# Optimization experiments

Hardware: AMD Instinct MI355X
Metric: run time of the kernel (lower is better)

## Reference

```python
import jax, jax.numpy as jnp
import numpy as np

B, IN, E, H, MO, OUT, K = 32768, 512, 8, 128, 256, 2, 2


def setup_inputs() -> dict:
    key = jax.random.key(0)
    ks = jax.random.split(key, 9)
    g = lambda k, shape, fan: (jax.random.normal(k, shape, jnp.float32) / np.sqrt(fan)).astype(jnp.float32)
    return {
        "num_prop": jax.random.normal(ks[0], (B, IN), jnp.float32),
        "cat_prop": jax.random.normal(ks[1], (B, 3), jnp.float32),
        "w_gate": g(ks[2], (IN, E), IN),
        "W1": g(ks[3], (E, IN, H), IN),
        "b1": jnp.zeros((E, H), jnp.float32),
        "W2": g(ks[4], (E, H, MO), H),
        "b2": jnp.zeros((E, MO), jnp.float32),
        "Wout": g(ks[5], (MO, OUT), MO),
        "bout": jnp.zeros((OUT,), jnp.float32),
    }


def _cv_squared(v):
    # torch.var is unbiased (ddof=1); eps = 1e-10
    return jnp.var(v, ddof=1) / (jnp.mean(v) ** 2 + 1e-10)


def reference(num_prop, cat_prop, w_gate, W1, b1, W2, b2, Wout, bout):
    b = num_prop.shape[0]
    x = num_prop  # eval mode: dropout is identity, gating noise disabled
    # --- top-k gating ---
    logits = x @ w_gate                                   # [B, E]
    top_vals, top_idx = jax.lax.top_k(logits, K)          # [B, K]
    gate_vals = jax.nn.softmax(top_vals, axis=-1)         # softmax over top-k logits
    gates = jnp.zeros_like(logits).at[jnp.arange(b)[:, None], top_idx].add(gate_vals)  # [B, E]
    # --- load-balancing loss ---
    importance = gates.sum(axis=0)                        # [E]
    load = (gates > 0).astype(jnp.float32).sum(axis=0)    # [E]
    loss = (_cv_squared(importance) + _cv_squared(load)) * 1e-2
    # --- experts (dense-equivalent: gates zero out non-selected experts) ---
    h = jax.nn.relu(jnp.einsum('bi,eih->beh', x, W1) + b1)          # [B, E, H]
    eo = jax.nn.softmax(jnp.einsum('beh,ehm->bem', h, W2) + b2, axis=-1)  # [B, E, MO]
    y = jnp.einsum('be,bem->bm', gates, eo)               # [B, MO]
    # --- output head ---
    out = y @ Wout + bout                                 # [B, OUT]
    return out, loss
```

## Files before the change

### kernel.cpp

```cpp
#include <hip/hip_runtime.h>

#define BN 32768
#define IN 512
#define NE 8
#define NH 128
#define MO 256

typedef const __attribute__((address_space(1))) unsigned int gu32;
typedef __attribute__((address_space(3))) unsigned int lu32;
typedef __attribute__((ext_vector_type(8))) short bf16x8;
typedef __attribute__((ext_vector_type(4))) float f32x4;

__device__ __forceinline__ void cp16(const float* g, float* l) {
    __builtin_amdgcn_global_load_lds((gu32*)g, (lu32*)l, 16, 0, 0);
}

__device__ __forceinline__ unsigned short f2bf(float f) {
    unsigned int u = __float_as_uint(f);
    u = (u + 0x7fffu + ((u >> 16) & 1u)) >> 16;
    return (unsigned short)u;
}
__device__ __forceinline__ float bf2f(unsigned short h) {
    return __uint_as_float((unsigned int)h << 16);
}

__global__ __launch_bounds__(256) void gate_kernel(
    const float* __restrict__ x, const float* __restrict__ wg,
    int* __restrict__ gcount, int* __restrict__ gload, float* __restrict__ gimp,
    int* __restrict__ idx_list, float* __restrict__ gate_list,
    float* __restrict__ out, const float* __restrict__ bout)
{
    __shared__ double wgt[NE][514];
    __shared__ int counts_s[NE];
    __shared__ int load_s[NE];
    __shared__ float imp_s[NE];
    __shared__ int base_s[NE];
    __shared__ int rec_e[64];
    __shared__ int rec_p[64];
    __shared__ float rec_g[64];

    int tid = threadIdx.x;
    if (tid < NE) { counts_s[tid] = 0; load_s[tid] = 0; imp_s[tid] = 0.f; }
    if (tid < 64) {
        int row = blockIdx.x * 32 + (tid >> 1);
        out[row * 2 + (tid & 1)] = bout[tid & 1];
    }
    for (int i = tid; i < IN * NE; i += 256) {
        wgt[i & 7][i >> 3] = (double)wg[i];
    }
    __syncthreads();

    int r = tid >> 3;
    int e = tid & 7;
    int row = blockIdx.x * 32 + r;

    const float4* x4 = (const float4*)(x + (size_t)row * IN);
    const double* wrow = &wgt[e][0];
    double a0 = 0.0, a1 = 0.0, a2 = 0.0, a3 = 0.0;
    #pragma unroll 8
    for (int j = 0; j < 128; ++j) {
        float4 xv = x4[j];
        const double2* wd = (const double2*)(wrow + 4 * j);
        double2 w0 = wd[0];
        double2 w1 = wd[1];
        a0 = fma((double)xv.x, w0.x, a0);
        a1 = fma((double)xv.y, w0.y, a1);
        a2 = fma((double)xv.z, w1.x, a2);
        a3 = fma((double)xv.w, w1.y, a3);
    }
    double acc = (a0 + a1) + (a2 + a3);

    double v0 = acc; int e0 = e;
    #pragma unroll
    for (int m = 1; m < 8; m <<= 1) {
        double vo = __shfl_xor(v0, m, 64);
        int    eo = __shfl_xor(e0, m, 64);
        if (vo > v0 || (vo == v0 && eo < e0)) { v0 = vo; e0 = eo; }
    }
    double v1 = (e == e0) ? -1.0e300 : acc; int e1 = e;
    #pragma unroll
    for (int m = 1; m < 8; m <<= 1) {
        double vo = __shfl_xor(v1, m, 64);
        int    eo = __shfl_xor(e1, m, 64);
        if (vo > v1 || (vo == v1 && eo < e1)) { v1 = vo; e1 = eo; }
    }

    if ((tid & 7) == 0) {
        float t1 = expf((float)(v1 - v0));
        float s = 1.f + t1;
        float g0 = 1.f / s;
        float g1 = t1 / s;
        atomicAdd(&imp_s[e0], g0);
        atomicAdd(&imp_s[e1], g1);
        if (g0 > 0.f) atomicAdd(&load_s[e0], 1);
        if (g1 > 0.f) atomicAdd(&load_s[e1], 1);
        int p0 = atomicAdd(&counts_s[e0], 1);
        int p1 = atomicAdd(&counts_s[e1], 1);
        int rl = r * 2;
        rec_e[rl] = e0; rec_e[rl + 1] = e1;
        rec_g[rl] = g0; rec_g[rl + 1] = g1;
        rec_p[rl] = p0; rec_p[rl + 1] = p1;
    }
    __syncthreads();
    if (tid < NE) {
        base_s[tid] = atomicAdd(&gcount[tid], counts_s[tid]);
        atomicAdd(&gimp[tid], imp_s[tid]);
        atomicAdd(&gload[tid], load_s[tid]);
    }
    __syncthreads();
    if (tid < 64) {
        int ee = rec_e[tid];
        int pos = base_s[ee] + rec_p[tid];
        int rw = blockIdx.x * 32 + (tid >> 1);
        idx_list[ee * BN + pos] = rw;
        gate_list[ee * BN + pos] = rec_g[tid];
    }
}

__global__ void loss_kernel(const float* __restrict__ gimp, const int* __restrict__ gload,
                            float* __restrict__ out) {
    if (threadIdx.x == 0 && blockIdx.x == 0) {
        float mi = 0.f, ml = 0.f;
        for (int e = 0; e < NE; ++e) { mi += gimp[e]; ml += (float)gload[e]; }
        mi *= 0.125f; ml *= 0.125f;
        float vi = 0.f, vl = 0.f;
        for (int e = 0; e < NE; ++e) {
            float d = gimp[e] - mi;  vi += d * d;
            float d2 = (float)gload[e] - ml; vl += d2 * d2;
        }
        vi *= (1.f / 7.f); vl *= (1.f / 7.f);
        float loss = (vi / (mi * mi + 1e-10f) + vl / (ml * ml + 1e-10f)) * 0.01f;
        out[BN * 2] = loss;
    }
}

__global__ __launch_bounds__(256) void prep_kernel(
    const float* __restrict__ W1, const float* __restrict__ W2,
    float* __restrict__ W1F, float* __restrict__ W2F)
{
    __shared__ __align__(16) char pb[32768];
    int t = threadIdx.x, b = blockIdx.x;
    if (b < 64) {
        int e = b >> 3, kt = b & 7;
        const float* src = W1 + ((size_t)e * IN + kt * 64) * NH;
        #pragma unroll
        for (int p = 0; p < 8; ++p) {
            int li = p * 256 + t;
            float4 q = *(const float4*)(src + li * 4);
            int kl = li >> 5, n0 = (li & 31) * 4;
            int ks = kl >> 5, g = (kl >> 3) & 3, kb = (kl & 7) * 2;
            float vv[4] = {q.x, q.y, q.z, q.w};
            #pragma unroll
            for (int j = 0; j < 4; ++j) {
                int n = n0 + j;
                int off = (((ks * 8 + (n >> 4)) * 64) + (n & 15) + 16 * g) * 16 + kb;
                unsigned short hh = f2bf(vv[j]);
                unsigned short hl = f2bf(vv[j] - bf2f(hh));
                *(unsigned short*)(pb + off) = hh;
                *(unsigned short*)(pb + 16384 + off) = hl;
            }
        }
        __syncthreads();
        float* dst = W1F + (size_t)b * 8192;
        #pragma unroll
        for (int p = 0; p < 8; ++p) {
            int li = p * 256 + t;
            *(int4*)(dst + li * 4) = *(const int4*)(pb + li * 16);
        }
    } else if (b < 96) {
        int bi = b - 64;
        int e = bi >> 2, kt = bi & 3;
        const float* src = W2 + ((size_t)e * NH + kt * 32) * MO;
        #pragma unroll
        for (int p = 0; p < 8; ++p) {
            int li = p * 256 + t;
            float4 q = *(const float4*)(src + li * 4);
            int kl = li >> 6, n0 = (li & 63) * 4;
            int g = kl >> 3, kb = (kl & 7) * 2;
            float vv[4] = {q.x, q.y, q.z, q.w};
            #pragma unroll
            for (int j = 0; j < 4; ++j) {
                int n = n0 + j;
                int off = ((n >> 4) * 64 + (n & 15) + 16 * g) * 16 + kb;
                unsigned short hh = f2bf(vv[j]);
                unsigned short hl = f2bf(vv[j] - bf2f(hh));
                *(unsigned short*)(pb + off) = hh;
                *(unsigned short*)(pb + 16384 + off) = hl;
            }
        }
        __syncthreads();
        float* dst = W2F + (size_t)bi * 8192;
        #pragma unroll
        for (int p = 0; p < 8; ++p) {
            int li = p * 256 + t;
            *(int4*)(dst + li * 4) = *(const int4*)(pb + li * 16);
        }
    }
}

#define OFF_AH 0
#define OFF_AL 8192
#define OFF_B1 16384
#define OFF_HH 0
#define OFF_HL 16384
#define OFF_B2 32768

__global__ __launch_bounds__(256, 2) void expert_kernel(
    const float* __restrict__ x,
    const float* __restrict__ b1, const float* __restrict__ b2,
    const float* __restrict__ Wout,
    const float* __restrict__ W1F, const float* __restrict__ W2F,
    const int* __restrict__ gcount,
    const int* __restrict__ idx_list, const float* __restrict__ gate_list,
    float* __restrict__ out)
{
    __shared__ __align__(16) char smx[66560];
    __shared__ float woutS[512];

    int e = blockIdx.y;
    int cnt = gcount[e];
    int row0 = blockIdx.x * 64;
    if (row0 >= cnt) return;
    int t = threadIdx.x;
    int l = t & 63, w = t >> 6;

    woutS[t] = Wout[t];
    woutS[256 + t] = Wout[256 + t];

    int s_mf = t >> 6;
    int s_r  = t & 15;
    int s_g  = (t >> 4) & 3;
    int rloc = s_mf * 16 + s_r;
    int sgi = row0 + rloc; if (sgi >= cnt) sgi = cnt - 1;
    const float* xrow = x + (size_t)idx_list[e * BN + sgi] * IN;

    int mbase = (w & 1) * 2;
    int nsel  = w >> 1;

    f32x4 acc1[2][4] = {};
    for (int kt = 0; kt < 8; ++kt) {
        {
            const float* gb = W1F + (size_t)(e * 8 + kt) * 8192;
            float* lb = (float*)(smx + OFF_B1);
            #pragma unroll
            for (int p = 0; p < 8; ++p)
                cp16(gb + (p * 256 + t) * 4, lb + (p * 256 + t) * 4);
        }
        #pragma unroll
        for (int ks = 0; ks < 2; ++ks) {
            int k = kt * 64 + ks * 32 + s_g * 8;
            float4 qa = *(const float4*)(xrow + k);
            float4 qb = *(const float4*)(xrow + k + 4);
            float vv[8] = {qa.x, qa.y, qa.z, qa.w, qb.x, qb.y, qb.z, qb.w};
            unsigned int dh[4], dl[4];
            #pragma unroll
            for (int j = 0; j < 4; ++j) {
                unsigned short h0 = f2bf(vv[2 * j]);
                unsigned short h1 = f2bf(vv[2 * j + 1]);
                unsigned short l0 = f2bf(vv[2 * j] - bf2f(h0));
                unsigned short l1 = f2bf(vv[2 * j + 1] - bf2f(h1));
                dh[j] = (unsigned int)h0 | ((unsigned int)h1 << 16);
                dl[j] = (unsigned int)l0 | ((unsigned int)l1 << 16);
            }
            int slot = ((ks * 4 + s_mf) * 64 + (s_r + 16 * s_g)) * 16;
            *(int4*)(smx + OFF_AH + slot) = make_int4(dh[0], dh[1], dh[2], dh[3]);
            *(int4*)(smx + OFF_AL + slot) = make_int4(dl[0], dl[1], dl[2], dl[3]);
        }
        __syncthreads();
        #pragma unroll
        for (int ks = 0; ks < 2; ++ks) {
            bf16x8 ah[2], al[2];
            #pragma unroll
            for (int mf = 0; mf < 2; ++mf) {
                int ao = ((ks * 4 + mbase + mf) * 64 + l) * 16;
                ah[mf] = *(const bf16x8*)(smx + OFF_AH + ao);
                al[mf] = *(const bf16x8*)(smx + OFF_AL + ao);
            }
            #pragma unroll
            for (int nf = 0; nf < 4; ++nf) {
                int bo = ((ks * 8 + nsel * 4 + nf) * 64 + l) * 16;
                bf16x8 bh = *(const bf16x8*)(smx + OFF_B1 + bo);
                bf16x8 bl = *(const bf16x8*)(smx + OFF_B1 + 16384 + bo);
                #pragma unroll
                for (int mf = 0; mf < 2; ++mf) {
                    acc1[mf][nf] = __builtin_amdgcn_mfma_f32_16x16x32_bf16(ah[mf], bh, acc1[mf][nf], 0, 0, 0);
                    acc1[mf][nf] = __builtin_amdgcn_mfma_f32_16x16x32_bf16(ah[mf], bl, acc1[mf][nf], 0, 0, 0);
                    acc1[mf][nf] = __builtin_amdgcn_mfma_f32_16x16x32_bf16(al[mf], bh, acc1[mf][nf], 0, 0, 0);
                    acc1[mf][nf] = __builtin_amdgcn_mfma_f32_16x16x32_bf16(al[mf], bl, acc1[mf][nf], 0, 0, 0);
                }
            }
        }
        __syncthreads();
    }

    #pragma unroll
    for (int mf = 0; mf < 2; ++mf) {
        int mf2 = (w & 1) * 2 + mf;
        int rlow = 4 * (l >> 4);
        #pragma unroll
        for (int nf = 0; nf < 4; ++nf) {
            int c = nsel * 64 + nf * 16 + (l & 15);
            float b1v = b1[e * NH + c];
            int ks2 = c >> 5;
            int g2 = (c >> 3) & 3;
            int boff = ((ks2 * 4 + mf2) * 64) * 16 + (c & 7) * 2;
            #pragma unroll
            for (int rg = 0; rg < 4; ++rg) {
                float v = fmaxf(acc1[mf][nf][rg] + b1v, 0.f);
                unsigned short hh = f2bf(v);
                unsigned short hl = f2bf(v - bf2f(hh));
                int off = boff + ((rlow + rg) + 16 * g2) * 16;
                *(unsigned short*)(smx + OFF_HH + off) = hh;
                *(unsigned short*)(smx + OFF_HL + off) = hl;
            }
        }
    }
    __syncthreads();

    f32x4 acc2[2][8] = {};
    for (int kt2 = 0; kt2 < 4; ++kt2) {
        {
            const float* gb = W2F + (size_t)(e * 4 + kt2) * 8192;
            float* lb = (float*)(smx + OFF_B2);
            #pragma unroll
            for (int p = 0; p < 8; ++p)
                cp16(gb + (p * 256 + t) * 4, lb + (p * 256 + t) * 4);
        }
        __syncthreads();
        bf16x8 ah[2], al[2];
        #pragma unroll
        for (int mf = 0; mf < 2; ++mf) {
            int ao = ((kt2 * 4 + mbase + mf) * 64 + l) * 16;
            ah[mf] = *(const bf16x8*)(smx + OFF_HH + ao);
            al[mf] = *(const bf16x8*)(smx + OFF_HL + ao);
        }
        #pragma unroll
        for (int nf = 0; nf < 8; ++nf) {
            int bo = ((nsel * 8 + nf) * 64 + l) * 16;
            bf16x8 bh = *(const bf16x8*)(smx + OFF_B2 + bo);
            bf16x8 bl = *(const bf16x8*)(smx + OFF_B2 + 16384 + bo);
            #pragma unroll
            for (int mf = 0; mf < 2; ++mf) {
                acc2[mf][nf] = __builtin_amdgcn_mfma_f32_16x16x32_bf16(ah[mf], bh, acc2[mf][nf], 0, 0, 0);
                acc2[mf][nf] = __builtin_amdgcn_mfma_f32_16x16x32_bf16(ah[mf], bl, acc2[mf][nf], 0, 0, 0);
                acc2[mf][nf] = __builtin_amdgcn_mfma_f32_16x16x32_bf16(al[mf], bh, acc2[mf][nf], 0, 0, 0);
                acc2[mf][nf] = __builtin_amdgcn_mfma_f32_16x16x32_bf16(al[mf], bl, acc2[mf][nf], 0, 0, 0);
            }
        }
        __syncthreads();
    }

    float* zl = (float*)smx;
    #pragma unroll
    for (int mf = 0; mf < 2; ++mf) {
        int rbase = (w & 1) * 32 + mf * 16 + 4 * (l >> 4);
        #pragma unroll
        for (int nf = 0; nf < 8; ++nf) {
            int c = nsel * 128 + nf * 16 + (l & 15);
            float b2v = b2[e * MO + c];
            #pragma unroll
            for (int rg = 0; rg < 4; ++rg)
                zl[(rbase + rg) * 260 + c] = acc2[mf][nf][rg] + b2v;
        }
    }
    __syncthreads();

    int rr = w * 16 + (l >> 2);
    int c0 = l & 3;
    float vreg[64];
    float m = -1e30f;
    #pragma unroll
    for (int j = 0; j < 64; ++j) {
        vreg[j] = zl[rr * 260 + c0 + 4 * j];
        m = fmaxf(m, vreg[j]);
    }
    m = fmaxf(m, __shfl_xor(m, 1, 64));
    m = fmaxf(m, __shfl_xor(m, 2, 64));
    float s = 0.f, o0 = 0.f, o1 = 0.f;
    #pragma unroll
    for (int j = 0; j < 64; ++j) {
        float tt = __expf(vreg[j] - m);
        s += tt;
        float2 wv = *(const float2*)&woutS[(c0 + 4 * j) * 2];
        o0 = fmaf(tt, wv.x, o0);
        o1 = fmaf(tt, wv.y, o1);
    }
    s  += __shfl_xor(s, 1, 64);  s  += __shfl_xor(s, 2, 64);
    o0 += __shfl_xor(o0, 1, 64); o0 += __shfl_xor(o0, 2, 64);
    o1 += __shfl_xor(o1, 1, 64); o1 += __shfl_xor(o1, 2, 64);
    if (c0 == 0) {
        int gi = row0 + rr;
        if (gi < cnt) {
            float g = gate_list[e * BN + gi];
            int brow = idx_list[e * BN + gi];
            float inv = 1.f / s;
            atomicAdd(&out[brow * 2 + 0], g * o0 * inv);
            atomicAdd(&out[brow * 2 + 1], g * o1 * inv);
        }
    }
}

extern "C" void kernel_launch(void* const* d_in, const int* in_sizes, int n_in,
                              void* d_out, int out_size, void* d_ws, size_t ws_size,
                              hipStream_t stream) {
    const float* x    = (const float*)d_in[0];
    const float* wg   = (const float*)d_in[2];
    const float* W1   = (const float*)d_in[3];
    const float* b1   = (const float*)d_in[4];
    const float* W2   = (const float*)d_in[5];
    const float* b2   = (const float*)d_in[6];
    const float* Wout = (const float*)d_in[7];
    const float* bout = (const float*)d_in[8];
    float* out = (float*)d_out;

    char* ws = (char*)d_ws;
    int*   gcount    = (int*)(ws + 0);
    int*   gload     = (int*)(ws + 32);
    float* gimp      = (float*)(ws + 64);
    int*   idx_list  = (int*)(ws + 128);
    float* gate_list = (float*)(ws + 128 + sizeof(int) * NE * BN);
    float* W1F       = (float*)(ws + 128 + 8 * NE * BN);
    float* W2F       = (float*)(ws + 128 + 8 * NE * BN + 64 * 32768);

    hipMemsetAsync(ws, 0, 128, stream);
    prep_kernel<<<96, 256, 0, stream>>>(W1, W2, W1F, W2F);
    gate_kernel<<<BN / 32, 256, 0, stream>>>(x, wg, gcount, gload, gimp,
                                             idx_list, gate_list, out, bout);
    loss_kernel<<<1, 64, 0, stream>>>(gimp, gload, out);
    dim3 eg(BN / 64, NE);
    expert_kernel<<<eg, 256, 0, stream>>>(x, b1, b2, Wout, W1F, W2F,
                                          gcount, idx_list, gate_list, out);
}
```

Measured before the change: 228.0 us.

## Rework gate precision, fuse loss into experts, double-buffer weights, register softmax

```diff
diff --git a/kernel.cpp b/kernel.cpp
--- a/kernel.cpp
+++ b/kernel.cpp
@@ -30,7 +30,7 @@
     int* __restrict__ idx_list, float* __restrict__ gate_list,
     float* __restrict__ out, const float* __restrict__ bout)
 {
-    __shared__ double wgt[NE][514];
+    __shared__ float wgs[NE][516];
     __shared__ int counts_s[NE];
     __shared__ int load_s[NE];
     __shared__ float imp_s[NE];
@@ -45,9 +45,7 @@
         int row = blockIdx.x * 32 + (tid >> 1);
         out[row * 2 + (tid & 1)] = bout[tid & 1];
     }
-    for (int i = tid; i < IN * NE; i += 256) {
-        wgt[i & 7][i >> 3] = (double)wg[i];
-    }
+    for (int i = tid; i < IN * NE; i += 256) wgs[i & 7][i >> 3] = wg[i];
     __syncthreads();
 
     int r = tid >> 3;
@@ -55,49 +53,78 @@
     int row = blockIdx.x * 32 + r;
 
     const float4* x4 = (const float4*)(x + (size_t)row * IN);
-    const double* wrow = &wgt[e][0];
-    double a0 = 0.0, a1 = 0.0, a2 = 0.0, a3 = 0.0;
+    float a0 = 0.f, a1 = 0.f, a2 = 0.f, a3 = 0.f;
     #pragma unroll 8
     for (int j = 0; j < 128; ++j) {
         float4 xv = x4[j];
-        const double2* wd = (const double2*)(wrow + 4 * j);
-        double2 w0 = wd[0];
-        double2 w1 = wd[1];
-        a0 = fma((double)xv.x, w0.x, a0);
-        a1 = fma((double)xv.y, w0.y, a1);
-        a2 = fma((double)xv.z, w1.x, a2);
-        a3 = fma((double)xv.w, w1.y, a3);
-    }
-    double acc = (a0 + a1) + (a2 + a3);
-
-    double v0 = acc; int e0 = e;
+        float4 wv = *(const float4*)&wgs[e][4 * j];
+        a0 = fmaf(xv.x, wv.x, a0);
+        a1 = fmaf(xv.y, wv.y, a1);
+        a2 = fmaf(xv.z, wv.z, a2);
+        a3 = fmaf(xv.w, wv.w, a3);
+    }
+    float acc = (a0 + a1) + (a2 + a3);
+
+    float v0 = acc; int e0 = e;
     #pragma unroll
     for (int m = 1; m < 8; m <<= 1) {
-        double vo = __shfl_xor(v0, m, 64);
-        int    eo = __shfl_xor(e0, m, 64);
+        float vo = __shfl_xor(v0, m, 64);
+        int eo = __shfl_xor(e0, m, 64);
         if (vo > v0 || (vo == v0 && eo < e0)) { v0 = vo; e0 = eo; }
     }
-    double v1 = (e == e0) ? -1.0e300 : acc; int e1 = e;
+    float v1 = (e == e0) ? -1e30f : acc; int e1 = e;
     #pragma unroll
     for (int m = 1; m < 8; m <<= 1) {
-        double vo = __shfl_xor(v1, m, 64);
-        int    eo = __shfl_xor(e1, m, 64);
+        float vo = __shfl_xor(v1, m, 64);
+        int eo = __shfl_xor(e1, m, 64);
         if (vo > v1 || (vo == v1 && eo < e1)) { v1 = vo; e1 = eo; }
     }
+    float v2 = (e == e0 || e == e1) ? -1e30f : acc;
+    #pragma unroll
+    for (int m = 1; m < 8; m <<= 1) v2 = fmaxf(v2, __shfl_xor(v2, m, 64));
+
+    double dv0 = v0, dv1 = v1;
+    int f0 = e0, f1 = e1;
+    if (v1 - v2 < 2e-4f) {
+        const float* xr = x + (size_t)row * IN;
+        double b0 = 0, b1d = 0, b2d = 0, b3 = 0;
+        for (int k = 0; k < IN; k += 4) {
+            b0  = fma((double)xr[k],     (double)wgs[e][k],     b0);
+            b1d = fma((double)xr[k + 1], (double)wgs[e][k + 1], b1d);
+            b2d = fma((double)xr[k + 2], (double)wgs[e][k + 2], b2d);
+            b3  = fma((double)xr[k + 3], (double)wgs[e][k + 3], b3);
+        }
+        double ad = (b0 + b1d) + (b2d + b3);
+        double w0 = ad; int g0i = e;
+        #pragma unroll
+        for (int m = 1; m < 8; m <<= 1) {
+            double vo = __shfl_xor(w0, m, 64);
+            int eo = __shfl_xor(g0i, m, 64);
+            if (vo > w0 || (vo == w0 && eo < g0i)) { w0 = vo; g0i = eo; }
+        }
+        double w1 = (e == g0i) ? -1.0e300 : ad; int g1i = e;
+        #pragma unroll
+        for (int m = 1; m < 8; m <<= 1) {
+            double vo = __shfl_xor(w1, m, 64);
+            int eo = __shfl_xor(g1i, m, 64);
+            if (vo > w1 || (vo == w1 && eo < g1i)) { w1 = vo; g1i = eo; }
+        }
+        dv0 = w0; dv1 = w1; f0 = g0i; f1 = g1i;
+    }
 
     if ((tid & 7) == 0) {
-        float t1 = expf((float)(v1 - v0));
+        float t1 = expf((float)(dv1 - dv0));
         float s = 1.f + t1;
         float g0 = 1.f / s;
         float g1 = t1 / s;
-        atomicAdd(&imp_s[e0], g0);
-        atomicAdd(&imp_s[e1], g1);
-        if (g0 > 0.f) atomicAdd(&load_s[e0], 1);
-        if (g1 > 0.f) atomicAdd(&load_s[e1], 1);
-        int p0 = atomicAdd(&counts_s[e0], 1);
-        int p1 = atomicAdd(&counts_s[e1], 1);
+        atomicAdd(&imp_s[f0], g0);
+        atomicAdd(&imp_s[f1], g1);
+        if (g0 > 0.f) atomicAdd(&load_s[f0], 1);
+        if (g1 > 0.f) atomicAdd(&load_s[f1], 1);
+        int p0 = atomicAdd(&counts_s[f0], 1);
+        int p1 = atomicAdd(&counts_s[f1], 1);
         int rl = r * 2;
-        rec_e[rl] = e0; rec_e[rl + 1] = e1;
+        rec_e[rl] = f0; rec_e[rl + 1] = f1;
         rec_g[rl] = g0; rec_g[rl + 1] = g1;
         rec_p[rl] = p0; rec_p[rl + 1] = p1;
     }
@@ -114,23 +141,6 @@
         int rw = blockIdx.x * 32 + (tid >> 1);
         idx_list[ee * BN + pos] = rw;
         gate_list[ee * BN + pos] = rec_g[tid];
-    }
-}
-
-__global__ void loss_kernel(const float* __restrict__ gimp, const int* __restrict__ gload,
-                            float* __restrict__ out) {
-    if (threadIdx.x == 0 && blockIdx.x == 0) {
-        float mi = 0.f, ml = 0.f;
-        for (int e = 0; e < NE; ++e) { mi += gimp[e]; ml += (float)gload[e]; }
-        mi *= 0.125f; ml *= 0.125f;
-        float vi = 0.f, vl = 0.f;
-        for (int e = 0; e < NE; ++e) {
-            float d = gimp[e] - mi;  vi += d * d;
-            float d2 = (float)gload[e] - ml; vl += d2 * d2;
-        }
-        vi *= (1.f / 7.f); vl *= (1.f / 7.f);
-        float loss = (vi / (mi * mi + 1e-10f) + vl / (ml * ml + 1e-10f)) * 0.01f;
-        out[BN * 2] = loss;
     }
 }
 
@@ -198,104 +208,118 @@
     }
 }
 
-#define OFF_AH 0
-#define OFF_AL 8192
-#define OFF_B1 16384
-#define OFF_HH 0
-#define OFF_HL 16384
-#define OFF_B2 32768
-
 __global__ __launch_bounds__(256, 2) void expert_kernel(
     const float* __restrict__ x,
     const float* __restrict__ b1, const float* __restrict__ b2,
     const float* __restrict__ Wout,
     const float* __restrict__ W1F, const float* __restrict__ W2F,
     const int* __restrict__ gcount,
+    const float* __restrict__ gimp, const int* __restrict__ gload,
     const int* __restrict__ idx_list, const float* __restrict__ gate_list,
     float* __restrict__ out)
 {
-    __shared__ __align__(16) char smx[66560];
+    __shared__ __align__(16) char buf0[32768];
+    __shared__ __align__(16) char buf1[32768];
     __shared__ float woutS[512];
+    __shared__ float redm[64][2];
+    __shared__ float red3[64][2][3];
 
     int e = blockIdx.y;
     int cnt = gcount[e];
     int row0 = blockIdx.x * 64;
+    if (e == 0 && blockIdx.x == 0 && threadIdx.x == 0) {
+        float mi = 0.f, ml = 0.f;
+        for (int k = 0; k < NE; ++k) { mi += gimp[k]; ml += (float)gload[k]; }
+        mi *= 0.125f; ml *= 0.125f;
+        float vi = 0.f, vl = 0.f;
+        for (int k = 0; k < NE; ++k) {
+            float d = gimp[k] - mi;  vi += d * d;
+            float d2 = (float)gload[k] - ml; vl += d2 * d2;
+        }
+        vi *= (1.f / 7.f); vl *= (1.f / 7.f);
+        out[BN * 2] = (vi / (mi * mi + 1e-10f) + vl / (ml * ml + 1e-10f)) * 0.01f;
+    }
     if (row0 >= cnt) return;
     int t = threadIdx.x;
     int l = t & 63, w = t >> 6;
+    int halfM = w & 1;
+    int nsel = w >> 1;
 
     woutS[t] = Wout[t];
     woutS[256 + t] = Wout[256 + t];
 
-    int s_mf = t >> 6;
-    int s_r  = t & 15;
-    int s_g  = (t >> 4) & 3;
-    int rloc = s_mf * 16 + s_r;
-    int sgi = row0 + rloc; if (sgi >= cnt) sgi = cnt - 1;
-    const float* xrow = x + (size_t)idx_list[e * BN + sgi] * IN;
-
-    int mbase = (w & 1) * 2;
-    int nsel  = w >> 1;
+    int rA = row0 + halfM * 32 + (l & 15);
+    int rB = rA + 16;
+    int iA = idx_list[e * BN + (rA < cnt ? rA : cnt - 1)];
+    int iB = idx_list[e * BN + (rB < cnt ? rB : cnt - 1)];
+    const float* pA = x + (size_t)iA * IN + 8 * (l >> 4);
+    const float* pB = x + (size_t)iB * IN + 8 * (l >> 4);
+
+    {
+        const float* gb = W1F + (size_t)(e * 8) * 8192;
+        float* lb = (float*)buf0;
+        #pragma unroll
+        for (int p = 0; p < 8; ++p)
+            cp16(gb + (p * 256 + t) * 4, lb + (p * 256 + t) * 4);
+    }
+    __syncthreads();
 
     f32x4 acc1[2][4] = {};
     for (int kt = 0; kt < 8; ++kt) {
+        float4 ra[2][2][2];
+        #pragma unroll
+        for (int mf = 0; mf < 2; ++mf) {
+            const float* pp = mf ? pB : pA;
+            #pragma unroll
+            for (int ks = 0; ks < 2; ++ks) {
+                ra[mf][ks][0] = *(const float4*)(pp + kt * 64 + ks * 32);
+                ra[mf][ks][1] = *(const float4*)(pp + kt * 64 + ks * 32 + 4);
+            }
+        }
         {
-            const float* gb = W1F + (size_t)(e * 8 + kt) * 8192;
-            float* lb = (float*)(smx + OFF_B1);
+            const float* gb = (kt < 7) ? (W1F + (size_t)(e * 8 + kt + 1) * 8192)
+                                       : (W2F + (size_t)(e * 4) * 8192);
+            float* lb = (float*)((kt & 1) ? buf0 : buf1);
             #pragma unroll
             for (int p = 0; p < 8; ++p)
                 cp16(gb + (p * 256 + t) * 4, lb + (p * 256 + t) * 4);
         }
-        #pragma unroll
-        for (int ks = 0; ks < 2; ++ks) {
-            int k = kt * 64 + ks * 32 + s_g * 8;
-            float4 qa = *(const float4*)(xrow + k);
-            float4 qb = *(const float4*)(xrow + k + 4);
-            float vv[8] = {qa.x, qa.y, qa.z, qa.w, qb.x, qb.y, qb.z, qb.w};
-            unsigned int dh[4], dl[4];
-            #pragma unroll
-            for (int j = 0; j < 4; ++j) {
-                unsigned short h0 = f2bf(vv[2 * j]);
-                unsigned short h1 = f2bf(vv[2 * j + 1]);
-                unsigned short l0 = f2bf(vv[2 * j] - bf2f(h0));
-                unsigned short l1 = f2bf(vv[2 * j + 1] - bf2f(h1));
-                dh[j] = (unsigned int)h0 | ((unsigned int)h1 << 16);
-                dl[j] = (unsigned int)l0 | ((unsigned int)l1 << 16);
-            }
-            int slot = ((ks * 4 + s_mf) * 64 + (s_r + 16 * s_g)) * 16;
-            *(int4*)(smx + OFF_AH + slot) = make_int4(dh[0], dh[1], dh[2], dh[3]);
-            *(int4*)(smx + OFF_AL + slot) = make_int4(dl[0], dl[1], dl[2], dl[3]);
-        }
-        __syncthreads();
-        #pragma unroll
-        for (int ks = 0; ks < 2; ++ks) {
-            bf16x8 ah[2], al[2];
-            #pragma unroll
-            for (int mf = 0; mf < 2; ++mf) {
-                int ao = ((ks * 4 + mbase + mf) * 64 + l) * 16;
-                ah[mf] = *(const bf16x8*)(smx + OFF_AH + ao);
-                al[mf] = *(const bf16x8*)(smx + OFF_AL + ao);
-            }
+        bf16x8 ah[2][2], al[2][2];
+        #pragma unroll
+        for (int mf = 0; mf < 2; ++mf)
+            #pragma unroll
+            for (int ks = 0; ks < 2; ++ks) {
+                float v[8] = {ra[mf][ks][0].x, ra[mf][ks][0].y, ra[mf][ks][0].z, ra[mf][ks][0].w,
+                              ra[mf][ks][1].x, ra[mf][ks][1].y, ra[mf][ks][1].z, ra[mf][ks][1].w};
+                #pragma unroll
+                for (int i = 0; i < 8; ++i) {
+                    unsigned short h = f2bf(v[i]);
+                    ah[mf][ks][i] = (short)h;
+                    al[mf][ks][i] = (short)f2bf(v[i] - bf2f(h));
+                }
+            }
+        const char* bb = (kt & 1) ? buf1 : buf0;
+        #pragma unroll
+        for (int ks = 0; ks < 2; ++ks)
             #pragma unroll
             for (int nf = 0; nf < 4; ++nf) {
                 int bo = ((ks * 8 + nsel * 4 + nf) * 64 + l) * 16;
-                bf16x8 bh = *(const bf16x8*)(smx + OFF_B1 + bo);
-                bf16x8 bl = *(const bf16x8*)(smx + OFF_B1 + 16384 + bo);
+                bf16x8 bh = *(const bf16x8*)(bb + bo);
+                bf16x8 bl = *(const bf16x8*)(bb + 16384 + bo);
                 #pragma unroll
                 for (int mf = 0; mf < 2; ++mf) {
-                    acc1[mf][nf] = __builtin_amdgcn_mfma_f32_16x16x32_bf16(ah[mf], bh, acc1[mf][nf], 0, 0, 0);
-                    acc1[mf][nf] = __builtin_amdgcn_mfma_f32_16x16x32_bf16(ah[mf], bl, acc1[mf][nf], 0, 0, 0);
-                    acc1[mf][nf] = __builtin_amdgcn_mfma_f32_16x16x32_bf16(al[mf], bh, acc1[mf][nf], 0, 0, 0);
-                    acc1[mf][nf] = __builtin_amdgcn_mfma_f32_16x16x32_bf16(al[mf], bl, acc1[mf][nf], 0, 0, 0);
+                    acc1[mf][nf] = __builtin_amdgcn_mfma_f32_16x16x32_bf16(ah[mf][ks], bh, acc1[mf][nf], 0, 0, 0);
+                    acc1[mf][nf] = __builtin_amdgcn_mfma_f32_16x16x32_bf16(ah[mf][ks], bl, acc1[mf][nf], 0, 0, 0);
+                    acc1[mf][nf] = __builtin_amdgcn_mfma_f32_16x16x32_bf16(al[mf][ks], bh, acc1[mf][nf], 0, 0, 0);
+                    acc1[mf][nf] = __builtin_amdgcn_mfma_f32_16x16x32_bf16(al[mf][ks], bl, acc1[mf][nf], 0, 0, 0);
                 }
             }
-        }
         __syncthreads();
     }
 
     #pragma unroll
     for (int mf = 0; mf < 2; ++mf) {
-        int mf2 = (w & 1) * 2 + mf;
+        int mf2 = halfM * 2 + mf;
         int rlow = 4 * (l >> 4);
         #pragma unroll
         for (int nf = 0; nf < 4; ++nf) {
@@ -310,93 +334,117 @@
                 unsigned short hh = f2bf(v);
                 unsigned short hl = f2bf(v - bf2f(hh));
                 int off = boff + ((rlow + rg) + 16 * g2) * 16;
-                *(unsigned short*)(smx + OFF_HH + off) = hh;
-                *(unsigned short*)(smx + OFF_HL + off) = hl;
-            }
-        }
-    }
-    __syncthreads();
+                *(unsigned short*)(buf1 + off) = hh;
+                *(unsigned short*)(buf1 + 16384 + off) = hl;
+            }
+        }
+    }
 
     f32x4 acc2[2][8] = {};
     for (int kt2 = 0; kt2 < 4; ++kt2) {
-        {
-            const float* gb = W2F + (size_t)(e * 4 + kt2) * 8192;
-            float* lb = (float*)(smx + OFF_B2);
+        __syncthreads();
+        bf16x8 ah2[2], al2[2];
+        #pragma unroll
+        for (int mf = 0; mf < 2; ++mf) {
+            int ao = ((kt2 * 4 + halfM * 2 + mf) * 64 + l) * 16;
+            ah2[mf] = *(const bf16x8*)(buf1 + ao);
+            al2[mf] = *(const bf16x8*)(buf1 + 16384 + ao);
+        }
+        #pragma unroll
+        for (int nf = 0; nf < 8; ++nf) {
+            int bo = ((nsel * 8 + nf) * 64 + l) * 16;
+            bf16x8 bh = *(const bf16x8*)(buf0 + bo);
+            bf16x8 bl = *(const bf16x8*)(buf0 + 16384 + bo);
+            #pragma unroll
+            for (int mf = 0; mf < 2; ++mf) {
+                acc2[mf][nf] = __builtin_amdgcn_mfma_f32_16x16x32_bf16(ah2[mf], bh, acc2[mf][nf], 0, 0, 0);
+                acc2[mf][nf] = __builtin_amdgcn_mfma_f32_16x16x32_bf16(ah2[mf], bl, acc2[mf][nf], 0, 0, 0);
+                acc2[mf][nf] = __builtin_amdgcn_mfma_f32_16x16x32_bf16(al2[mf], bh, acc2[mf][nf], 0, 0, 0);
+                acc2[mf][nf] = __builtin_amdgcn_mfma_f32_16x16x32_bf16(al2[mf], bl, acc2[mf][nf], 0, 0, 0);
+            }
+        }
+        if (kt2 < 3) {
+            __syncthreads();
+            const float* gb = W2F + (size_t)(e * 4 + kt2 + 1) * 8192;
+            float* lb = (float*)buf0;
             #pragma unroll
             for (int p = 0; p < 8; ++p)
                 cp16(gb + (p * 256 + t) * 4, lb + (p * 256 + t) * 4);
         }
-        __syncthreads();
-        bf16x8 ah[2], al[2];
-        #pragma unroll
-        for (int mf = 0; mf < 2; ++mf) {
-            int ao = ((kt2 * 4 + mbase + mf) * 64 + l) * 16;
-            ah[mf] = *(const bf16x8*)(smx + OFF_HH + ao);
-            al[mf] = *(const bf16x8*)(smx + OFF_HL + ao);
-        }
-        #pragma unroll
-        for (int nf = 0; nf < 8; ++nf) {
-            int bo = ((nsel * 8 + nf) * 64 + l) * 16;
-            bf16x8 bh = *(const bf16x8*)(smx + OFF_B2 + bo);
-            bf16x8 bl = *(const bf16x8*)(smx + OFF_B2 + 16384 + bo);
-            #pragma unroll
-            for (int mf = 0; mf < 2; ++mf) {
-                acc2[mf][nf] = __builtin_amdgcn_mfma_f32_16x16x32_bf16(ah[mf], bh, acc2[mf][nf], 0, 0, 0);
-                acc2[mf][nf] = __builtin_amdgcn_mfma_f32_16x16x32_bf16(ah[mf], bl, acc2[mf][nf], 0, 0, 0);
-                acc2[mf][nf] = __builtin_amdgcn_mfma_f32_16x16x32_bf16(al[mf], bh, acc2[mf][nf], 0, 0, 0);
-                acc2[mf][nf] = __builtin_amdgcn_mfma_f32_16x16x32_bf16(al[mf], bl, acc2[mf][nf], 0, 0, 0);
-            }
-        }
-        __syncthreads();
-    }
-
-    float* zl = (float*)smx;
-    #pragma unroll
-    for (int mf = 0; mf < 2; ++mf) {
-        int rbase = (w & 1) * 32 + mf * 16 + 4 * (l >> 4);
-        #pragma unroll
-        for (int nf = 0; nf < 8; ++nf) {
-            int c = nsel * 128 + nf * 16 + (l & 15);
-            float b2v = b2[e * MO + c];
-            #pragma unroll
-            for (int rg = 0; rg < 4; ++rg)
-                zl[(rbase + rg) * 260 + c] = acc2[mf][nf][rg] + b2v;
-        }
-    }
-    __syncthreads();
-
-    int rr = w * 16 + (l >> 2);
-    int c0 = l & 3;
-    float vreg[64];
-    float m = -1e30f;
-    #pragma unroll
-    for (int j = 0; j < 64; ++j) {
-        vreg[j] = zl[rr * 260 + c0 + 4 * j];
-        m = fmaxf(m, vreg[j]);
-    }
-    m = fmaxf(m, __shfl_xor(m, 1, 64));
-    m = fmaxf(m, __shfl_xor(m, 2, 64));
-    float s = 0.f, o0 = 0.f, o1 = 0.f;
-    #pragma unroll
-    for (int j = 0; j < 64; ++j) {
-        float tt = __expf(vreg[j] - m);
-        s += tt;
-        float2 wv = *(const float2*)&woutS[(c0 + 4 * j) * 2];
-        o0 = fmaf(tt, wv.x, o0);
-        o1 = fmaf(tt, wv.y, o1);
-    }
-    s  += __shfl_xor(s, 1, 64);  s  += __shfl_xor(s, 2, 64);
-    o0 += __shfl_xor(o0, 1, 64); o0 += __shfl_xor(o0, 2, 64);
-    o1 += __shfl_xor(o1, 1, 64); o1 += __shfl_xor(o1, 2, 64);
-    if (c0 == 0) {
-        int gi = row0 + rr;
-        if (gi < cnt) {
-            float g = gate_list[e * BN + gi];
-            int brow = idx_list[e * BN + gi];
-            float inv = 1.f / s;
-            atomicAdd(&out[brow * 2 + 0], g * o0 * inv);
-            atomicAdd(&out[brow * 2 + 1], g * o1 * inv);
-        }
+    }
+
+    float2 wrow[8];
+    #pragma unroll
+    for (int nf = 0; nf < 8; ++nf) {
+        int c = nsel * 128 + nf * 16 + (l & 15);
+        float b2v = b2[e * MO + c];
+        #pragma unroll
+        for (int rg = 0; rg < 4; ++rg) {
+            acc2[0][nf][rg] += b2v;
+            acc2[1][nf][rg] += b2v;
+        }
+        wrow[nf] = *(const float2*)&woutS[2 * c];
+    }
+    #pragma unroll
+    for (int mf = 0; mf < 2; ++mf)
+        #pragma unroll
+        for (int rg = 0; rg < 4; ++rg) {
+            float m = -1e30f;
+            #pragma unroll
+            for (int nf = 0; nf < 8; ++nf) m = fmaxf(m, acc2[mf][nf][rg]);
+            m = fmaxf(m, __shfl_xor(m, 1, 64));
+            m = fmaxf(m, __shfl_xor(m, 2, 64));
+            m = fmaxf(m, __shfl_xor(m, 4, 64));
+            m = fmaxf(m, __shfl_xor(m, 8, 64));
+            int rloc = halfM * 32 + mf * 16 + 4 * (l >> 4) + rg;
+            if ((l & 15) == 0) redm[rloc][nsel] = m;
+        }
+    __syncthreads();
+    #pragma unroll
+    for (int mf = 0; mf < 2; ++mf)
+        #pragma unroll
+        for (int rg = 0; rg < 4; ++rg) {
+            int rloc = halfM * 32 + mf * 16 + 4 * (l >> 4) + rg;
+            float M = fmaxf(redm[rloc][0], redm[rloc][1]);
+            float s = 0.f, o0 = 0.f, o1 = 0.f;
+            #pragma unroll
+            for (int nf = 0; nf < 8; ++nf) {
+                float tt = __expf(acc2[mf][nf][rg] - M);
+                s += tt;
+                o0 = fmaf(tt, wrow[nf].x, o0);
+                o1 = fmaf(tt, wrow[nf].y, o1);
+            }
+            s += __shfl_xor(s, 1, 64); s += __shfl_xor(s, 2, 64);
+            s += __shfl_xor(s, 4, 64); s += __shfl_xor(s, 8, 64);
+            o0 += __shfl_xor(o0, 1, 64); o0 += __shfl_xor(o0, 2, 64);
+            o0 += __shfl_xor(o0, 4, 64); o0 += __shfl_xor(o0, 8, 64);
+            o1 += __shfl_xor(o1, 1, 64); o1 += __shfl_xor(o1, 2, 64);
+            o1 += __shfl_xor(o1, 4, 64); o1 += __shfl_xor(o1, 8, 64);
+            if ((l & 15) == 0) {
+                red3[rloc][nsel][0] = s;
+                red3[rloc][nsel][1] = o0;
+                red3[rloc][nsel][2] = o1;
+            }
+        }
+    __syncthreads();
+    if (nsel == 0 && (l & 15) == 0) {
+        #pragma unroll
+        for (int mf = 0; mf < 2; ++mf)
+            #pragma unroll
+            for (int rg = 0; rg < 4; ++rg) {
+                int rloc = halfM * 32 + mf * 16 + 4 * (l >> 4) + rg;
+                float S  = red3[rloc][0][0] + red3[rloc][1][0];
+                float O0 = red3[rloc][0][1] + red3[rloc][1][1];
+                float O1 = red3[rloc][0][2] + red3[rloc][1][2];
+                int gi = row0 + rloc;
+                if (gi < cnt) {
+                    float g = gate_list[e * BN + gi];
+                    int brow = idx_list[e * BN + gi];
+                    float inv = 1.f / S;
+                    atomicAdd(&out[brow * 2 + 0], g * O0 * inv);
+                    atomicAdd(&out[brow * 2 + 1], g * O1 * inv);
+                }
+            }
     }
 }
 
@@ -426,8 +474,8 @@
     prep_kernel<<<96, 256, 0, stream>>>(W1, W2, W1F, W2F);
     gate_kernel<<<BN / 32, 256, 0, stream>>>(x, wg, gcount, gload, gimp,
                                              idx_list, gate_list, out, bout);
-    loss_kernel<<<1, 64, 0, stream>>>(gimp, gload, out);
     dim3 eg(BN / 64, NE);
     expert_kernel<<<eg, 256, 0, stream>>>(x, b1, b2, Wout, W1F, W2F,
-                                          gcount, idx_list, gate_list, out);
-}
+                                          gcount, gimp, gload,
+                                          idx_list, gate_list, out);
+}
```

After: 250.6 us. +9.9%, slower.
